# Kernel tuning notes

Hardware: AMD Instinct MI355X
Metric: run time of the kernel (lower is better)

## Reference

```python
import jax, jax.numpy as jnp
import numpy as np

N = 50000      # nodes
E = 800000     # edges (avg degree 16)
D = 128        # input_nf = output_nf
H = 128        # hidden_nf


def _lin_init(key, fan_in, fan_out, gain=1.0):
    return gain * jax.random.normal(key, (fan_in, fan_out), jnp.float32) / np.sqrt(fan_in)


def setup_inputs() -> dict:
    key = jax.random.key(0)
    ks = jax.random.split(key, 20)
    h = jax.random.normal(ks[0], (N, D), jnp.float32)
    coord_diff = 0.5 * jax.random.normal(ks[1], (E, 3), jnp.float32)
    row = jax.random.randint(ks[2], (E,), 0, N, jnp.int32)
    col = jax.random.randint(ks[3], (E,), 0, N, jnp.int32)
    return {
        "h": h, "coord_diff": coord_diff, "row": row, "col": col,
        # edge_nn: Linear(2D+1 -> H), SiLU, Linear(H -> H), SiLU
        "We1": _lin_init(ks[4], 2 * D + 1, H), "be1": jnp.zeros((H,), jnp.float32),
        "We2": _lin_init(ks[5], H, H),          "be2": jnp.zeros((H,), jnp.float32),
        # node_nn: Linear(H+D -> H), SiLU, Linear(H -> D)
        "Wn1": _lin_init(ks[6], H + D, H), "bn1": jnp.zeros((H,), jnp.float32),
        "Wn2": _lin_init(ks[7], H, D),     "bn2": jnp.zeros((D,), jnp.float32),
        # coord_nn: Linear(H -> H), SiLU, Linear(H -> 1, no bias, gain 0.001)
        "Wc1": _lin_init(ks[8], H, H), "bc1": jnp.zeros((H,), jnp.float32),
        "Wc2": _lin_init(ks[9], H, 1, gain=0.001),
        # vel_scaling_nn: Linear(D -> H), SiLU, Linear(H -> 1)
        "Wv1": _lin_init(ks[10], D, H), "bv1": jnp.zeros((H,), jnp.float32),
        "Wv2": _lin_init(ks[11], H, 1), "bv2": jnp.zeros((1,), jnp.float32),
    }


def reference(h, coord_diff, row, col,
              We1, be1, We2, be2,
              Wn1, bn1, Wn2, bn2,
              Wc1, bc1, Wc2,
              Wv1, bv1, Wv2, bv2):
    n = h.shape[0]
    silu = jax.nn.silu
    # radial: squared edge length, [E,1]
    radial = jnp.sum(coord_diff * coord_diff, axis=1, keepdims=True)
    # edge model: gather endpoint features + radial, 2-layer SiLU MLP
    e_in = jnp.concatenate([h[row], h[col], radial], axis=1)        # [E, 2D+1]
    m = silu(silu(e_in @ We1 + be1) @ We2 + be2)                    # [E, H]
    # force model: per-edge scalar coefficient, clamped scatter-mean (coords_weight=1.0)
    coef = silu(m @ Wc1 + bc1) @ Wc2                                # [E, 1]
    trans = jnp.clip(coord_diff * coef, -100.0, 100.0)              # [E, 3]
    f_sum = jax.ops.segment_sum(trans, row, num_segments=n)         # [N, 3]
    cnt = jax.ops.segment_sum(jnp.ones((trans.shape[0], 1), trans.dtype), row, num_segments=n)
    force = f_sum / jnp.clip(cnt, 1.0)                              # segment mean, count clamped >=1
    # node model: scatter-sum of edge messages, then 2-layer MLP
    agg = jax.ops.segment_sum(m, row, num_segments=n)               # [N, H]
    h_cat = jnp.concatenate([h, agg], axis=1)                       # [N, D+H]
    h_out = silu(h_cat @ Wn1 + bn1) @ Wn2 + bn2                     # [N, D]
    # velocity scaling head
    vel = silu(h @ Wv1 + bv1) @ Wv2 + bv2                           # [N, 1]
    return (vel, force, h_out)
```

## Files before the change

kernel.cpp:

```cpp
#include <hip/hip_runtime.h>

#define NN 50000
#define EE 800000
#define PGB ((NN + 31) / 32)

typedef unsigned short u16;
typedef unsigned int u32;
typedef __attribute__((ext_vector_type(8))) short short8;
typedef __attribute__((ext_vector_type(4))) float f32x4;
typedef __attribute__((ext_vector_type(2))) float f32x2;

__device__ __forceinline__ u16 f2bf(float f) {
    union { float f; u32 i; } v; v.f = f;
    u32 x = v.i;
    return (u16)((x + 0x7fffu + ((x >> 16) & 1u)) >> 16);
}
__device__ __forceinline__ u32 pkr(float lo, float hi) {
    union { float f; u32 i; } a, b; a.f = lo; b.f = hi;
    return __builtin_amdgcn_perm(b.i + 0x8000u, a.i + 0x8000u, 0x07060302u);
}
__device__ __forceinline__ float bf2f(short x) {
    union { u32 i; float f; } v; v.i = ((u32)(u16)x) << 16; return v.f;
}
__device__ __forceinline__ float siluf(float x) {
    return x * __builtin_amdgcn_rcpf(1.0f + __expf(-x));
}
__device__ __forceinline__ void atomic_pk_add_bf16(u16* addr, u32 data) {
    asm volatile("global_atomic_pk_add_bf16 %0, %1, off" :: "v"(addr), "v"(data) : "memory");
}

__device__ __forceinline__ int b_idx2(int k, int n) {
    int chunk = ((k >> 5) << 3) + ((n >> 5) << 1) + (n & 1);
    return chunk * 512 + (((k >> 3) & 3) << 7) + (((n >> 1) & 15) << 3) + (k & 7);
}

__global__ __launch_bounds__(256) void prephist_kernel(
    const float* __restrict__ We1, const float* __restrict__ We2,
    const float* __restrict__ Wc1, const float* __restrict__ Wn1,
    const float* __restrict__ Wn2, const float* __restrict__ Wv1,
    u16* __restrict__ We1bf, u16* __restrict__ We2bf, u16* __restrict__ Wc1bf,
    u16* __restrict__ Wn1bf, u16* __restrict__ Wn2bf, u16* __restrict__ Wv1bf,
    const int* __restrict__ row, u32* __restrict__ bins,
    u32* __restrict__ rank, u32 use_ext)
{
    if (blockIdx.x >= 512) {
        int e = (blockIdx.x - 512) * 256 + threadIdx.x;
        if (e < EE) {
            u32 rk = atomicAdd(&bins[row[e]], 1u);
            if (use_ext) rank[e] = rk;
        }
        return;
    }
    int i = blockIdx.x * 256 + threadIdx.x;
    if (i < 32768) {
        int k = i >> 7, n = i & 127;
        We1bf[b_idx2(k, n)] = f2bf(We1[k * 128 + n]);
    } else if (i < 49152) {
        int t = i - 32768; int k = t >> 7, n = t & 127;
        We2bf[b_idx2(k, n)] = f2bf(We2[k * 128 + n]);
    } else if (i < 65536) {
        int t = i - 49152; int k = t >> 7, n = t & 127;
        Wc1bf[b_idx2(k, n)] = f2bf(Wc1[k * 128 + n]);
    } else if (i < 98304) {
        int t = i - 65536; int k = t >> 7, n = t & 127;
        Wn1bf[b_idx2(k, n)] = f2bf(Wn1[k * 128 + n]);
    } else if (i < 114688) {
        int t = i - 98304; int k = t >> 7, n = t & 127;
        Wn2bf[b_idx2(k, n)] = f2bf(Wn2[k * 128 + n]);
    } else {
        int t = i - 114688; int k = t >> 7, n = t & 127;
        Wv1bf[b_idx2(k, n)] = f2bf(Wv1[k * 128 + n]);
    }
}

__global__ __launch_bounds__(256) void scan1_kernel(const u32* __restrict__ bins,
                                                    u32* __restrict__ part)
{
    __shared__ u32 wsum[4];
    int i = blockIdx.x * 256 + threadIdx.x;
    u32 v = (i < NN) ? bins[i] : 0u;
    #pragma unroll
    for (int o = 1; o < 64; o <<= 1) v += __shfl_xor(v, o);
    if ((threadIdx.x & 63) == 0) wsum[threadIdx.x >> 6] = v;
    __syncthreads();
    if (threadIdx.x == 0) part[blockIdx.x] = wsum[0] + wsum[1] + wsum[2] + wsum[3];
}

__global__ __launch_bounds__(256) void scan3_kernel(const u32* __restrict__ bins,
                                                    const u32* __restrict__ part,
                                                    u32* __restrict__ cursor, int np)
{
    __shared__ u32 sPart[256];
    __shared__ u32 wsum[4];
    int t = threadIdx.x;
    sPart[t] = (t < np) ? part[t] : 0u;
    __syncthreads();
    if (t == 0) {
        u32 run = 0;
        for (int i = 0; i < np; ++i) { u32 x = sPart[i]; sPart[i] = run; run += x; }
    }
    int i = blockIdx.x * 256 + t;
    u32 v = (i < NN) ? bins[i] : 0u;
    u32 x = v;
    #pragma unroll
    for (int o = 1; o < 64; o <<= 1) {
        u32 y = __shfl_up(x, o);
        if ((t & 63) >= o) x += y;
    }
    if ((t & 63) == 63) wsum[t >> 6] = x;
    __syncthreads();
    u32 base = sPart[blockIdx.x];
    for (int wv = 0; wv < (t >> 6); ++wv) base += wsum[wv];
    if (i < NN) cursor[i] = base + x - v;
}

__global__ __launch_bounds__(256, 4) void pgemm_scatter_kernel(
    const float* __restrict__ h, const float* __restrict__ be1,
    const float* __restrict__ bv1, const float* __restrict__ Wv2,
    const float* __restrict__ bv2,
    const u16* __restrict__ We1bf, const u16* __restrict__ Wv1bf,
    u16* __restrict__ P1bf, u16* __restrict__ P2bf,
    u16* __restrict__ hbf, u32 use_ext, float* __restrict__ vel,
    const int* __restrict__ row, const int* __restrict__ col,
    const float* __restrict__ cdiff, u32* __restrict__ cursor,
    const u32* __restrict__ rank, u32* __restrict__ edata)
{
    __shared__ u16 sX[4096];
    __shared__ float sVelP[4][32];

    if (blockIdx.x >= PGB) {
        int e = (blockIdx.x - PGB) * 256 + threadIdx.x;
        if (e < EE) {
            int r = row[e];
            u32 p = use_ext ? (cursor[r] + rank[e]) : atomicAdd(&cursor[r], 1u);
            float cx = cdiff[(size_t)e * 3 + 0];
            float cy = cdiff[(size_t)e * 3 + 1];
            float cz = cdiff[(size_t)e * 3 + 2];
            float rad = cx * cx + cy * cy + cz * cz;
            uint4 ed;
            ed.x = (u32)r;
            ed.y = (u32)col[e];
            ed.z = __float_as_uint(rad);
            ed.w = (u32)e;
            *(uint4*)(edata + (size_t)p * 4) = ed;
        }
        return;
    }

    const int tid = threadIdx.x;
    const int nblk = blockIdx.x * 32;
    const int w = tid >> 6;
    const int lane = tid & 63;
    const int m15 = lane & 15, q = lane >> 4;
    const int n0 = w * 32 + 2 * m15, n1 = n0 + 1;
    const int ard = (m15 + 32 * q) * 8;
    const float b0 = be1[n0], b1 = be1[n1];

    {
        int r = tid & 31, j = tid >> 5;
        int n = nblk + r; if (n > NN - 1) n = NN - 1;
        #pragma unroll
        for (int i = 0; i < 2; ++i) {
            int kg = j * 2 + i;
            const float* src = h + (size_t)n * 128 + kg * 8;
            float4 a = *(const float4*)(src);
            float4 b = *(const float4*)(src + 4);
            uint4 v = make_uint4(pkr(a.x, a.y), pkr(a.z, a.w),
                                 pkr(b.x, b.y), pkr(b.z, b.w));
            *(uint4*)&sX[(r + 32 * kg) * 8] = v;
            if (use_ext)
                *(uint4*)(hbf + (size_t)n * 128 + kg * 8) = v;
        }
    }
    __syncthreads();

    f32x4 acc[2][2];

    #pragma unroll
    for (int mt = 0; mt < 2; ++mt)
        #pragma unroll
        for (int r = 0; r < 4; ++r) { acc[mt][0][r] = b0; acc[mt][1][r] = b1; }
    #pragma unroll
    for (int c = 0; c < 4; ++c) {
        short8 bf0 = *(const short8*)(We1bf + (c * 8 + w * 2 + 0) * 512 + lane * 8);
        short8 bf1 = *(const short8*)(We1bf + (c * 8 + w * 2 + 1) * 512 + lane * 8);
        #pragma unroll
        for (int mt = 0; mt < 2; ++mt) {
            short8 af = *(const short8*)(sX + ard + c * 1024 + mt * 128);
            acc[mt][0] = __builtin_amdgcn_mfma_f32_16x16x32_bf16(af, bf0, acc[mt][0], 0, 0, 0);
            acc[mt][1] = __builtin_amdgcn_mfma_f32_16x16x32_bf16(af, bf1, acc[mt][1], 0, 0, 0);
        }
    }
    #pragma unroll
    for (int mt = 0; mt < 2; ++mt)
        #pragma unroll
        for (int r = 0; r < 4; ++r) {
            int n = nblk + mt * 16 + q * 4 + r;
            if (n < NN)
                *(u32*)(P1bf + (size_t)n * 128 + n0) = pkr(acc[mt][0][r], acc[mt][1][r]);
        }

    #pragma unroll
    for (int mt = 0; mt < 2; ++mt)
        #pragma unroll
        for (int r = 0; r < 4; ++r) { acc[mt][0][r] = 0.0f; acc[mt][1][r] = 0.0f; }
    #pragma unroll
    for (int c = 4; c < 8; ++c) {
        short8 bf0 = *(const short8*)(We1bf + (c * 8 + w * 2 + 0) * 512 + lane * 8);
        short8 bf1 = *(const short8*)(We1bf + (c * 8 + w * 2 + 1) * 512 + lane * 8);
        #pragma unroll
        for (int mt = 0; mt < 2; ++mt) {
            short8 af = *(const short8*)(sX + ard + (c - 4) * 1024 + mt * 128);
            acc[mt][0] = __builtin_amdgcn_mfma_f32_16x16x32_bf16(af, bf0, acc[mt][0], 0, 0, 0);
            acc[mt][1] = __builtin_amdgcn_mfma_f32_16x16x32_bf16(af, bf1, acc[mt][1], 0, 0, 0);
        }
    }
    #pragma unroll
    for (int mt = 0; mt < 2; ++mt)
        #pragma unroll
        for (int r = 0; r < 4; ++r) {
            int n = nblk + mt * 16 + q * 4 + r;
            if (n < NN)
                *(u32*)(P2bf + (size_t)n * 128 + n0) = pkr(acc[mt][0][r], acc[mt][1][r]);
        }

    {
        const float bva = bv1[n0], bvb = bv1[n1];
        const float wv2a = Wv2[n0], wv2b = Wv2[n1];
        #pragma unroll
        for (int mt = 0; mt < 2; ++mt)
            #pragma unroll
            for (int r = 0; r < 4; ++r) { acc[mt][0][r] = bva; acc[mt][1][r] = bvb; }
        #pragma unroll
        for (int c = 0; c < 4; ++c) {
            short8 bf0 = *(const short8*)(Wv1bf + (c * 8 + w * 2 + 0) * 512 + lane * 8);
            short8 bf1 = *(const short8*)(Wv1bf + (c * 8 + w * 2 + 1) * 512 + lane * 8);
            #pragma unroll
            for (int mt = 0; mt < 2; ++mt) {
                short8 af = *(const short8*)(sX + ard + c * 1024 + mt * 128);
                acc[mt][0] = __builtin_amdgcn_mfma_f32_16x16x32_bf16(af, bf0, acc[mt][0], 0, 0, 0);
                acc[mt][1] = __builtin_amdgcn_mfma_f32_16x16x32_bf16(af, bf1, acc[mt][1], 0, 0, 0);
            }
        }
        #pragma unroll
        for (int mt = 0; mt < 2; ++mt)
            #pragma unroll
            for (int r = 0; r < 4; ++r) {
                float pv = fmaf(siluf(acc[mt][0][r]), wv2a, siluf(acc[mt][1][r]) * wv2b);
                pv += __shfl_xor(pv, 1);
                pv += __shfl_xor(pv, 2);
                pv += __shfl_xor(pv, 4);
                pv += __shfl_xor(pv, 8);
                if (m15 == 0) sVelP[w][mt * 16 + q * 4 + r] = pv;
            }
        __syncthreads();
        if (tid < 32) {
            int n = nblk + tid;
            if (n < NN)
                vel[n] = bv2[0] + sVelP[0][tid] + sVelP[1][tid] + sVelP[2][tid] + sVelP[3][tid];
        }
    }
}

__global__ __launch_bounds__(256, 8) void edge_kernel(
    const u16* __restrict__ P1bf, const u16* __restrict__ P2bf,
    const float* __restrict__ cdiff,
    const u32* __restrict__ edata,
    const float* __restrict__ We1,
    const float* __restrict__ be2, const float* __restrict__ bc1,
    const float* __restrict__ Wc2,
    const u16* __restrict__ We2bf, const u16* __restrict__ Wc1bf,
    u16* __restrict__ aggbf, float* __restrict__ fsum)
{
    __shared__ u16 sT[8192];
    __shared__ int sRow[64];
    __shared__ int sEg[64];
    __shared__ int sRid[64];
    __shared__ float sCoefP[4][64];
    __shared__ float sF[192];

    const int tid = threadIdx.x;
    const int e0 = blockIdx.x * 64;
    const int w = tid >> 6;
    const int lane = tid & 63;
    const int m15 = lane & 15, q = lane >> 4;
    const int n0 = w * 32 + 2 * m15, n1 = n0 + 1;
    const int lsw = (lane ^ q) * 8;
    const int a_ = m15 >> 2;
    const int sbase = (a_ << 7) + (q << 5) + ((m15 & 3) << 1);
    const int o0 = (0 ^ a_) << 3, o1 = (1 ^ a_) << 3, o2 = (2 ^ a_) << 3, o3 = (3 ^ a_) << 3;

    const float b2a = be2[n0], b2b = be2[n1];
    const float b3a = bc1[n0], b3b = bc1[n1];
    const float wc2a = Wc2[n0], wc2b = Wc2[n1];

    {
        int e = tid & 63, seg = tid >> 6;
        uint4 ed = *(const uint4*)(edata + (size_t)(e0 + e) * 4);
        int nr = (int)ed.x, nc = (int)ed.y;
        float rad = __uint_as_float(ed.z);
        if (seg == 0) { sRow[e] = nr; sEg[e] = (int)ed.w; }
        const u16* p1 = P1bf + (size_t)nr * 128 + seg * 32;
        const u16* p2 = P2bf + (size_t)nc * 128 + seg * 32;
        const float* wr = We1 + 256 * 128 + seg * 32;
        u16* tb = sT + (((seg * 4 + (e >> 4)) << 9) + (((e >> 2) & 3) << 5));
        const int rl = e & 3;
        #pragma unroll 2
        for (int g = 0; g < 4; ++g) {
            short8 x1 = *(const short8*)(p1 + g * 8);
            short8 x2 = *(const short8*)(p2 + g * 8);
            float4 wa = *(const float4*)(wr + g * 8);
            float4 wb = *(const float4*)(wr + g * 8 + 4);
            float v[8];
            #pragma unroll
            for (int t = 0; t < 4; ++t) {
                v[t]     = siluf(bf2f(x1[t])     + bf2f(x2[t])     + rad * ((const float*)&wa)[t]);
                v[t + 4] = siluf(bf2f(x1[t + 4]) + bf2f(x2[t + 4]) + rad * ((const float*)&wb)[t]);
            }
            uint4 dd = make_uint4(pkr(v[0], v[1]), pkr(v[2], v[3]),
                                  pkr(v[4], v[5]), pkr(v[6], v[7]));
            *(uint4*)(tb + ((g << 7) + ((rl ^ g) << 3))) = dd;
        }
    }
    __syncthreads();

    if (tid < 64) {
        int e = tid;
        int head = (e == 0) || (sRow[e] != sRow[e - 1]);
        int v = head ? e : 0;
        #pragma unroll
        for (int o = 1; o < 64; o <<= 1) {
            int y = __shfl_up(v, o);
            if (e >= o && y > v) v = y;
        }
        sRid[e] = v;
        sF[e * 3 + 0] = 0.f; sF[e * 3 + 1] = 0.f; sF[e * 3 + 2] = 0.f;
    }

    f32x4 acc[4][2];
    u32 d[4][4];

    #pragma unroll
    for (int mt = 0; mt < 4; ++mt)
        #pragma unroll
        for (int r = 0; r < 4; ++r) { acc[mt][0][r] = b2a; acc[mt][1][r] = b2b; }
    #pragma unroll
    for (int c = 0; c < 4; ++c) {
        short8 bf0 = *(const short8*)(We2bf + (c * 8 + w * 2 + 0) * 512 + lane * 8);
        short8 bf1 = *(const short8*)(We2bf + (c * 8 + w * 2 + 1) * 512 + lane * 8);
        #pragma unroll
        for (int mt = 0; mt < 4; ++mt) {
            short8 af = *(const short8*)(sT + (c * 4 + mt) * 512 + lsw);
            acc[mt][0] = __builtin_amdgcn_mfma_f32_16x16x32_bf16(af, bf0, acc[mt][0], 0, 0, 0);
            acc[mt][1] = __builtin_amdgcn_mfma_f32_16x16x32_bf16(af, bf1, acc[mt][1], 0, 0, 0);
        }
    }
    #pragma unroll
    for (int mt = 0; mt < 4; ++mt)
        #pragma unroll
        for (int r = 0; r < 4; ++r)
            d[mt][r] = pkr(siluf(acc[mt][0][r]), siluf(acc[mt][1][r]));
    __syncthreads();
    #pragma unroll
    for (int mt = 0; mt < 4; ++mt) {
        u16* bp = sT + (w * 4 + mt) * 512 + sbase;
        *(u32*)(bp + o0) = d[mt][0];
        *(u32*)(bp + o1) = d[mt][1];
        *(u32*)(bp + o2) = d[mt][2];
        *(u32*)(bp + o3) = d[mt][3];
    }
    __syncthreads();

    #pragma unroll
    for (int mt = 0; mt < 4; ++mt)
        #pragma unroll
        for (int r = 0; r < 4; ++r) { acc[mt][0][r] = b3a; acc[mt][1][r] = b3b; }
    #pragma unroll
    for (int c = 0; c < 4; ++c) {
        short8 bf0 = *(const short8*)(Wc1bf + (c * 8 + w * 2 + 0) * 512 + lane * 8);
        short8 bf1 = *(const short8*)(Wc1bf + (c * 8 + w * 2 + 1) * 512 + lane * 8);
        #pragma unroll
        for (int mt = 0; mt < 4; ++mt) {
            short8 af = *(const short8*)(sT + (c * 4 + mt) * 512 + lsw);
            acc[mt][0] = __builtin_amdgcn_mfma_f32_16x16x32_bf16(af, bf0, acc[mt][0], 0, 0, 0);
            acc[mt][1] = __builtin_amdgcn_mfma_f32_16x16x32_bf16(af, bf1, acc[mt][1], 0, 0, 0);
        }
    }
    #pragma unroll
    for (int mt = 0; mt < 4; ++mt)
        #pragma unroll
        for (int r = 0; r < 4; ++r) {
            float pv = fmaf(siluf(acc[mt][0][r]), wc2a, siluf(acc[mt][1][r]) * wc2b);
            pv += __shfl_xor(pv, 1);
            pv += __shfl_xor(pv, 2);
            pv += __shfl_xor(pv, 4);
            pv += __shfl_xor(pv, 8);
            if (m15 == 0) sCoefP[w][mt * 16 + q * 4 + r] = pv;
        }

    {
        const int P = tid & 63, C = 2 * P, g = tid >> 6;
        const int xorb = (C >> 3) & 3;
        const int base = ((((C >> 5) * 4 + g) << 9)) + (((C >> 3) & 3) << 7) + (C & 7);
        float s0 = 0.f, s1 = 0.f;
        int prow = sRow[g * 16];
        #pragma unroll
        for (int i = 0; i < 16; ++i) {
            u32 v = *(const u32*)(sT + base + (((i >> 2) & 3) << 5) + (((i & 3) ^ xorb) << 3));
            int r = sRow[g * 16 + i];
            if (r != prow) {
                atomic_pk_add_bf16(aggbf + (size_t)prow * 128 + C, pkr(s0, s1));
                s0 = 0.f; s1 = 0.f; prow = r;
            }
            s0 += bf2f((short)(v & 0xffffu));
            s1 += bf2f((short)(v >> 16));
        }
        atomic_pk_add_bf16(aggbf + (size_t)prow * 128 + C, pkr(s0, s1));
    }
    __syncthreads();

    if (tid < 192) {
        int e = tid / 3, ax = tid - e * 3;
        float coef = sCoefP[0][e] + sCoefP[1][e] + sCoefP[2][e] + sCoefP[3][e];
        float tr = cdiff[(size_t)sEg[e] * 3 + ax] * coef;
        tr = fminf(fmaxf(tr, -100.f), 100.f);
        atomicAdd(&sF[sRid[e] * 3 + ax], tr);
    }
    __syncthreads();
    if (tid < 192) {
        int e = tid / 3, ax = tid - e * 3;
        if (e == 0 || sRow[e] != sRow[e - 1])
            atomicAdd(&fsum[(size_t)sRow[e] * 3 + ax], sF[e * 3 + ax]);
    }
}

__global__ __launch_bounds__(256, 4) void node_kernel(
    const float* __restrict__ h, const u16* __restrict__ hbf, u32 use_ext,
    const float* __restrict__ bn1, const float* __restrict__ bn2,
    const u16* __restrict__ Wn1bf, const u16* __restrict__ Wn2bf,
    const u16* __restrict__ aggbf, const float* __restrict__ fsum,
    const u32* __restrict__ bins, float* __restrict__ out)
{
    __shared__ u16 sX[8192];
    __shared__ float sBn1[128], sBn2[128];
    u16* sT = sX + 4096;

    const int tid = threadIdx.x;
    const int nblk = blockIdx.x * 32;
    const int w = tid >> 6;
    const int lane = tid & 63;
    const int m15 = lane & 15, q = lane >> 4;
    const int n0 = w * 32 + 2 * m15, n1 = n0 + 1;
    const int lsw = (lane ^ q) * 8;
    const int a_ = m15 >> 2;
    const int sbase = (a_ << 7) + (q << 5) + ((m15 & 3) << 1);
    const int o0 = (0 ^ a_) << 3, o1 = (1 ^ a_) << 3, o2 = (2 ^ a_) << 3, o3 = (3 ^ a_) << 3;
    const int ard = (m15 + 32 * q) * 8;

    if (tid < 96) {
        int r = tid / 3, ax = tid - r * 3;
        int n = nblk + r;
        if (n < NN)
            out[NN + (size_t)n * 3 + ax] = fsum[(size_t)n * 3 + ax] * __builtin_amdgcn_rcpf(fmaxf((float)bins[n], 1.0f));
    }
    if (tid < 128) { sBn1[tid] = bn1[tid]; sBn2[tid] = bn2[tid]; }

    {
        int r = tid & 31, j = tid >> 5;
        int n = nblk + r; if (n > NN - 1) n = NN - 1;
        if (j < 4) {
            if (use_ext) {
                #pragma unroll
                for (int i = 0; i < 4; ++i) {
                    int kg = j * 4 + i;
                    *(uint4*)&sX[(r + 32 * kg) * 8] =
                        *(const uint4*)(hbf + (size_t)n * 128 + kg * 8);
                }
            } else {
                #pragma unroll
                for (int i = 0; i < 4; ++i) {
                    int kg = j * 4 + i;
                    const float* src = h + (size_t)n * 128 + kg * 8;
                    float4 a = *(const float4*)(src);
                    float4 b = *(const float4*)(src + 4);
                    *(uint4*)&sX[(r + 32 * kg) * 8] = make_uint4(pkr(a.x, a.y), pkr(a.z, a.w),
                                                                 pkr(b.x, b.y), pkr(b.z, b.w));
                }
            }
        } else {
            #pragma unroll
            for (int i = 0; i < 4; ++i) {
                int kg = j * 4 + i;
                *(uint4*)&sX[(r + 32 * kg) * 8] =
                    *(const uint4*)(aggbf + (size_t)n * 128 + (kg - 16) * 8);
            }
        }
    }
    __syncthreads();

    f32x4 acc[2][2];

    {
        float b0 = sBn1[n0], b1 = sBn1[n1];
        #pragma unroll
        for (int mt = 0; mt < 2; ++mt)
            #pragma unroll
            for (int r = 0; r < 4; ++r) { acc[mt][0][r] = b0; acc[mt][1][r] = b1; }
    }
    #pragma unroll
    for (int c = 0; c < 8; ++c) {
        short8 bf0 = *(const short8*)(Wn1bf + (c * 8 + w * 2 + 0) * 512 + lane * 8);
        short8 bf1 = *(const short8*)(Wn1bf + (c * 8 + w * 2 + 1) * 512 + lane * 8);
        #pragma unroll
        for (int mt = 0; mt < 2; ++mt) {
            short8 af = *(const short8*)(sX + ard + c * 1024 + mt * 128);
            acc[mt][0] = __builtin_amdgcn_mfma_f32_16x16x32_bf16(af, bf0, acc[mt][0], 0, 0, 0);
            acc[mt][1] = __builtin_amdgcn_mfma_f32_16x16x32_bf16(af, bf1, acc[mt][1], 0, 0, 0);
        }
    }
    u32 dn[2][4];
    #pragma unroll
    for (int mt = 0; mt < 2; ++mt)
        #pragma unroll
        for (int r = 0; r < 4; ++r)
            dn[mt][r] = pkr(siluf(acc[mt][0][r]), siluf(acc[mt][1][r]));
    __syncthreads();
    #pragma unroll
    for (int mt = 0; mt < 2; ++mt) {
        u16* bp = sT + (w * 2 + mt) * 512 + sbase;
        *(u32*)(bp + o0) = dn[mt][0];
        *(u32*)(bp + o1) = dn[mt][1];
        *(u32*)(bp + o2) = dn[mt][2];
        *(u32*)(bp + o3) = dn[mt][3];
    }
    __syncthreads();

    {
        float b0 = sBn2[n0], b1 = sBn2[n1];
        #pragma unroll
        for (int mt = 0; mt < 2; ++mt)
            #pragma unroll
            for (int r = 0; r < 4; ++r) { acc[mt][0][r] = b0; acc[mt][1][r] = b1; }
    }
    #pragma unroll
    for (int c = 0; c < 4; ++c) {
        short8 bf0 = *(const short8*)(Wn2bf + (c * 8 + w * 2 + 0) * 512 + lane * 8);
        short8 bf1 = *(const short8*)(Wn2bf + (c * 8 + w * 2 + 1) * 512 + lane * 8);
        #pragma unroll
        for (int mt = 0; mt < 2; ++mt) {
            short8 af = *(const short8*)(sT + (c * 2 + mt) * 512 + lsw);
            acc[mt][0] = __builtin_amdgcn_mfma_f32_16x16x32_bf16(af, bf0, acc[mt][0], 0, 0, 0);
            acc[mt][1] = __builtin_amdgcn_mfma_f32_16x16x32_bf16(af, bf1, acc[mt][1], 0, 0, 0);
        }
    }
    #pragma unroll
    for (int mt = 0; mt < 2; ++mt)
        #pragma unroll
        for (int r = 0; r < 4; ++r) {
            int n = nblk + mt * 16 + q * 4 + r;
            if (n < NN) {
                f32x2 v; v.x = acc[mt][0][r]; v.y = acc[mt][1][r];
                *(f32x2*)(out + (size_t)4 * NN + (size_t)n * 128 + n0) = v;
            }
        }
}

extern "C" void kernel_launch(void* const* d_in, const int* in_sizes, int n_in,
                              void* d_out, int out_size, void* d_ws, size_t ws_size,
                              hipStream_t stream) {
    const float* h     = (const float*)d_in[0];
    const float* cdiff = (const float*)d_in[1];
    const int* row     = (const int*)d_in[2];
    const int* col     = (const int*)d_in[3];
    const float* We1 = (const float*)d_in[4];
    const float* be1 = (const float*)d_in[5];
    const float* We2 = (const float*)d_in[6];
    const float* be2 = (const float*)d_in[7];
    const float* Wn1 = (const float*)d_in[8];
    const float* bn1 = (const float*)d_in[9];
    const float* Wn2 = (const float*)d_in[10];
    const float* bn2 = (const float*)d_in[11];
    const float* Wc1 = (const float*)d_in[12];
    const float* bc1 = (const float*)d_in[13];
    const float* Wc2 = (const float*)d_in[14];
    const float* Wv1 = (const float*)d_in[15];
    const float* bv1 = (const float*)d_in[16];
    const float* Wv2 = (const float*)d_in[17];
    const float* bv2 = (const float*)d_in[18];

    u16* aggbf  = (u16*)d_ws;
    float* fsum = (float*)(aggbf + (size_t)NN * 128);
    u32* bins   = (u32*)(fsum + (size_t)NN * 3);
    u16* We1bf = (u16*)(bins + NN);
    u16* We2bf = We1bf + 32768;
    u16* Wc1bf = We2bf + 16384;
    u16* Wn1bf = Wc1bf + 16384;
    u16* Wn2bf = Wn1bf + 32768;
    u16* Wv1bf = Wn2bf + 16384;
    u16* P1bf  = Wv1bf + 16384;
    float* out = (float*)d_out;

    const size_t base_bytes = (size_t)26662144;
    u16* hbf  = (u16*)((char*)d_ws + base_bytes);
    u32* rank = (u32*)((char*)d_ws + base_bytes + (size_t)NN * 256);
    u32 use_ext = (ws_size >= base_bytes + (size_t)NN * 256 + (size_t)EE * 4) ? 1u : 0u;

    u32* cursor = (u32*)(out + NN);
    u32* part   = cursor + NN;
    u16* P2bf   = (u16*)(out + (size_t)4 * NN);
    u32* edata  = (u32*)(P2bf + (size_t)NN * 128);

    size_t zero_bytes = (size_t)NN * 128 * 2 + (size_t)NN * 3 * 4 + (size_t)NN * 4;
    hipMemsetAsync(d_ws, 0, zero_bytes, stream);

    const int NSC = (NN + 255) / 256;

    prephist_kernel<<<512 + (EE + 255) / 256, 256, 0, stream>>>(
        We1, We2, Wc1, Wn1, Wn2, Wv1,
        We1bf, We2bf, Wc1bf, Wn1bf, Wn2bf, Wv1bf,
        row, bins, rank, use_ext);
    scan1_kernel<<<NSC, 256, 0, stream>>>(bins, part);
    scan3_kernel<<<NSC, 256, 0, stream>>>(bins, part, cursor, NSC);
    pgemm_scatter_kernel<<<PGB + (EE + 255) / 256, 256, 0, stream>>>(
        h, be1, bv1, Wv2, bv2,
        We1bf, Wv1bf, P1bf, P2bf,
        hbf, use_ext, out,
        row, col, cdiff, cursor, rank, edata);
    edge_kernel<<<EE / 64, 256, 0, stream>>>(P1bf, P2bf, cdiff, edata,
                                             We1, be2, bc1, Wc2,
                                             We2bf, Wc1bf,
                                             aggbf, fsum);
    node_kernel<<<(NN + 31) / 32, 256, 0, stream>>>(h, hbf, use_ext,
                                                    bn1, bn2,
                                                    Wn1bf, Wn2bf,
                                                    aggbf, fsum, bins, out);
}
```

Baseline: 341.7 us.

## Fuse message aggregation into layer-2 epilogue and remap blocks per XCD

```diff
diff --git a/kernel.cpp b/kernel.cpp
--- a/kernel.cpp
+++ b/kernel.cpp
@@ -280,7 +280,10 @@
     __shared__ float sF[192];
 
     const int tid = threadIdx.x;
-    const int e0 = blockIdx.x * 64;
+    const int xcd = blockIdx.x & 7, off = blockIdx.x >> 3;
+    const int qq = 12500 >> 3, rr = 12500 & 7;
+    const int lb = (xcd < rr ? xcd * (qq + 1) : rr * (qq + 1) + (xcd - rr) * qq) + off;
+    const int e0 = lb * 64;
     const int w = tid >> 6;
     const int lane = tid & 63;
     const int m15 = lane & 15, q = lane >> 4;
@@ -356,10 +359,23 @@
         }
     }
     #pragma unroll
-    for (int mt = 0; mt < 4; ++mt)
-        #pragma unroll
-        for (int r = 0; r < 4; ++r)
-            d[mt][r] = pkr(siluf(acc[mt][0][r]), siluf(acc[mt][1][r]));
+    for (int mt = 0; mt < 4; ++mt) {
+        float s0 = 0.f, s1 = 0.f;
+        int prow = sRow[mt * 16 + q * 4];
+        #pragma unroll
+        for (int r = 0; r < 4; ++r) {
+            int rr2 = sRow[mt * 16 + q * 4 + r];
+            float sl0 = siluf(acc[mt][0][r]);
+            float sl1 = siluf(acc[mt][1][r]);
+            d[mt][r] = pkr(sl0, sl1);
+            if (rr2 != prow) {
+                atomic_pk_add_bf16(aggbf + (size_t)prow * 128 + n0, pkr(s0, s1));
+                s0 = 0.f; s1 = 0.f; prow = rr2;
+            }
+            s0 += sl0; s1 += sl1;
+        }
+        atomic_pk_add_bf16(aggbf + (size_t)prow * 128 + n0, pkr(s0, s1));
+    }
     __syncthreads();
     #pragma unroll
     for (int mt = 0; mt < 4; ++mt) {
@@ -397,26 +413,6 @@
             pv += __shfl_xor(pv, 8);
             if (m15 == 0) sCoefP[w][mt * 16 + q * 4 + r] = pv;
         }
-
-    {
-        const int P = tid & 63, C = 2 * P, g = tid >> 6;
-        const int xorb = (C >> 3) & 3;
-        const int base = ((((C >> 5) * 4 + g) << 9)) + (((C >> 3) & 3) << 7) + (C & 7);
-        float s0 = 0.f, s1 = 0.f;
-        int prow = sRow[g * 16];
-        #pragma unroll
-        for (int i = 0; i < 16; ++i) {
-            u32 v = *(const u32*)(sT + base + (((i >> 2) & 3) << 5) + (((i & 3) ^ xorb) << 3));
-            int r = sRow[g * 16 + i];
-            if (r != prow) {
-                atomic_pk_add_bf16(aggbf + (size_t)prow * 128 + C, pkr(s0, s1));
-                s0 = 0.f; s1 = 0.f; prow = r;
-            }
-            s0 += bf2f((short)(v & 0xffffu));
-            s1 += bf2f((short)(v >> 16));
-        }
-        atomic_pk_add_bf16(aggbf + (size_t)prow * 128 + C, pkr(s0, s1));
-    }
     __syncthreads();
 
     if (tid < 192) {
```

After: 446.0 us. +30.5%, slower.
